# Kernel optimization log

Measured on AMD Instinct MI355X. Metric: run time of the kernel, lower is better.

The kernel has to match this reference:

```python
import jax, jax.numpy as jnp
import numpy as np

TOP_K = 8  # config.top_k


def setup_inputs() -> dict:
    key = jax.random.key(0)
    k1, k2 = jax.random.split(key)
    B, S, H, E = 4, 4096, 4096, 64
    x = jax.random.normal(k1, (B, S, H), dtype=jnp.float32)
    # nn.Linear(hidden_size, expert_num, bias=False) weight: [E, H]
    W = jax.random.normal(k2, (E, H), dtype=jnp.float32) / np.sqrt(H).astype(np.float32)
    return {"x": x, "W": W}


def reference(x, W):
    # gate linear: [B,S,H] @ [E,H]^T -> [B,S,E]
    logits = jnp.einsum('bsh,eh->bse', x, W)
    # top-k along experts
    topk_vals, indices = jax.lax.top_k(logits, TOP_K)  # [B,S,K]
    # scatter topk values into a -inf-filled tensor. Since the scattered src
    # values are exactly the logits at those indices, this equals masking.
    E = logits.shape[-1]
    mask = jax.nn.one_hot(indices, E, dtype=bool).any(axis=-2)  # [B,S,E]
    sparse_logits = jnp.where(mask, logits, -jnp.inf)
    sparse_probs = jax.nn.softmax(sparse_logits, axis=-1)  # [B,S,E]
    gate_logit = logits.reshape(-1, E)  # [B*S, E]
    return sparse_probs, indices, gate_logit
```

## Files before the change

### kernel.cpp

```cpp
#include <hip/hip_runtime.h>
#include <math.h>

#define H_DIM  4096
#define E_NUM  64
#define N_TOK  16384
#define TPB    64
#define KC     64
#define NCHUNK (H_DIM / KC)
#define TOPK   8

#define N_PROBS  (N_TOK * E_NUM)
#define N_IDX    (N_TOK * TOPK)
#define OFF_IDX  N_PROBS
#define OFF_GATE (N_PROBS + N_IDX)

__global__ __launch_bounds__(256, 1)
void gating_kernel(const float* __restrict__ x, const float* __restrict__ W,
                   float* __restrict__ out) {
  __shared__ union {
    float xs[2][KC][TPB];
    float lg[TPB][E_NUM + 1];
  } u;
  __shared__ float ws[2][KC][E_NUM];

  const int tid  = threadIdx.x;
  const int tok0 = blockIdx.x * TPB;
  const int tx   = tid & 15;
  const int ty   = tid >> 4;

  const float* xg = x + (size_t)tok0 * H_DIM;

  float4 xr[4], wr[4];

  auto gload = [&](int kb) {
#pragma unroll
    for (int p = 0; p < 4; ++p) {
      const int f4  = tid + 256 * p;
      const int row = f4 & 63;
      const int kq  = f4 >> 6;
      xr[p] = *(const float4*)(xg + row * H_DIM + kb + 4 * kq);
      wr[p] = *(const float4*)(W  + row * H_DIM + kb + 4 * kq);
    }
  };
  auto sstore = [&](int b) {
#pragma unroll
    for (int p = 0; p < 4; ++p) {
      const int f4  = tid + 256 * p;
      const int row = f4 & 63;
      const int k0  = (f4 >> 6) << 2;
      u.xs[b][k0 + 0][row] = xr[p].x;
      u.xs[b][k0 + 1][row] = xr[p].y;
      u.xs[b][k0 + 2][row] = xr[p].z;
      u.xs[b][k0 + 3][row] = xr[p].w;
      ws[b][k0 + 0][row] = wr[p].x;
      ws[b][k0 + 1][row] = wr[p].y;
      ws[b][k0 + 2][row] = wr[p].z;
      ws[b][k0 + 3][row] = wr[p].w;
    }
  };

  gload(0);
  sstore(0);
  __syncthreads();

  double accd[4][4];
#pragma unroll
  for (int i = 0; i < 4; ++i)
#pragma unroll
    for (int j = 0; j < 4; ++j) accd[i][j] = 0.0;

  for (int c = 0; c < NCHUNK; ++c) {
    if (c + 1 < NCHUNK) gload((c + 1) * KC);
    const int b = c & 1;

    float ca[4][4];
#pragma unroll
    for (int i = 0; i < 4; ++i)
#pragma unroll
      for (int j = 0; j < 4; ++j) ca[i][j] = 0.f;

#pragma unroll 8
    for (int k = 0; k < KC; ++k) {
      const float4 av = *(const float4*)&u.xs[b][k][4 * ty];
      const float4 bv = *(const float4*)&ws[b][k][4 * tx];
      const float a[4]  = {av.x, av.y, av.z, av.w};
      const float bb[4] = {bv.x, bv.y, bv.z, bv.w};
#pragma unroll
      for (int i = 0; i < 4; ++i)
#pragma unroll
        for (int j = 0; j < 4; ++j)
          ca[i][j] = fmaf(a[i], bb[j], ca[i][j]);
    }
#pragma unroll
    for (int i = 0; i < 4; ++i)
#pragma unroll
      for (int j = 0; j < 4; ++j) accd[i][j] += (double)ca[i][j];

    if (c + 1 < NCHUNK) {
      sstore((c + 1) & 1);
      __syncthreads();
    }
  }

  float acc[4][4];
#pragma unroll
  for (int i = 0; i < 4; ++i)
#pragma unroll
    for (int j = 0; j < 4; ++j) acc[i][j] = (float)accd[i][j];

  float* gate = out + OFF_GATE;
#pragma unroll
  for (int i = 0; i < 4; ++i) {
    const int t = 4 * ty + i;
    float4 v = make_float4(acc[i][0], acc[i][1], acc[i][2], acc[i][3]);
    *(float4*)(gate + (size_t)(tok0 + t) * E_NUM + 4 * tx) = v;
  }

  __syncthreads();
#pragma unroll
  for (int i = 0; i < 4; ++i)
#pragma unroll
    for (int j = 0; j < 4; ++j)
      u.lg[4 * ty + i][4 * tx + j] = acc[i][j];
  __syncthreads();

  if (tid < TPB) {
    const int t = tid;
    float vals[TOPK];
    int   idxs[TOPK];
#pragma unroll
    for (int p = 0; p < TOPK; ++p) {
      float best = -INFINITY;
      int   bi   = 0;
      for (int e = 0; e < E_NUM; ++e) {
        const float v = u.lg[t][e];
        if (v > best) { best = v; bi = e; }
      }
      vals[p] = best;
      idxs[p] = bi;
      u.lg[t][bi] = -INFINITY;
    }
    const float m = vals[0];
    float s = 0.f, pr[TOPK];
#pragma unroll
    for (int p = 0; p < TOPK; ++p) { pr[p] = __expf(vals[p] - m); s += pr[p]; }
    const float inv = 1.0f / s;
    for (int e = 0; e < E_NUM; ++e) u.lg[t][e] = 0.f;
#pragma unroll
    for (int p = 0; p < TOPK; ++p) u.lg[t][idxs[p]] = pr[p] * inv;

    float* oidx = out + OFF_IDX + (size_t)(tok0 + t) * TOPK;
#pragma unroll
    for (int p = 0; p < TOPK; ++p) oidx[p] = (float)idxs[p];
  }
  __syncthreads();

  float* oprob = out + (size_t)tok0 * E_NUM;
#pragma unroll
  for (int p = 0; p < 16; ++p) {
    const int f = tid + 256 * p;
    oprob[f] = u.lg[f >> 6][f & 63];
  }
}

extern "C" void kernel_launch(void* const* d_in, const int* in_sizes, int n_in,
                              void* d_out, int out_size, void* d_ws, size_t ws_size,
                              hipStream_t stream) {
  const float* x = (const float*)d_in[0];
  const float* W = (const float*)d_in[1];
  float* out = (float*)d_out;
  dim3 grid(N_TOK / TPB);
  dim3 block(256);
  gating_kernel<<<grid, block, 0, stream>>>(x, W, out);
}
```

Measured before the change: 453.7 us.

## Split K across two thread groups per block and reduce partials in shared memory

```diff
diff --git a/kernel.cpp b/kernel.cpp
--- a/kernel.cpp
+++ b/kernel.cpp
@@ -14,28 +14,30 @@
 #define OFF_IDX  N_PROBS
 #define OFF_GATE (N_PROBS + N_IDX)
 
-__global__ __launch_bounds__(256, 1)
+__global__ __launch_bounds__(512, 2)
 void gating_kernel(const float* __restrict__ x, const float* __restrict__ W,
                    float* __restrict__ out) {
   __shared__ union {
-    float xs[2][KC][TPB];
+    struct { float xs[2][KC][TPB]; float ws[2][KC][E_NUM]; } t;
+    struct { float pad[8192]; double b[16][256]; } r;
     float lg[TPB][E_NUM + 1];
   } u;
-  __shared__ float ws[2][KC][E_NUM];
 
   const int tid  = threadIdx.x;
+  const int g    = tid >> 8;
+  const int gtid = tid & 255;
   const int tok0 = blockIdx.x * TPB;
-  const int tx   = tid & 15;
-  const int ty   = tid >> 4;
+  const int tx   = gtid & 15;
+  const int ty   = gtid >> 4;
 
   const float* xg = x + (size_t)tok0 * H_DIM;
 
-  float4 xr[4], wr[4];
+  float4 xr[2], wr[2];
 
   auto gload = [&](int kb) {
 #pragma unroll
-    for (int p = 0; p < 4; ++p) {
-      const int f4  = tid + 256 * p;
+    for (int p = 0; p < 2; ++p) {
+      const int f4  = tid + 512 * p;
       const int row = f4 & 63;
       const int kq  = f4 >> 6;
       xr[p] = *(const float4*)(xg + row * H_DIM + kb + 4 * kq);
@@ -44,18 +46,18 @@
   };
   auto sstore = [&](int b) {
 #pragma unroll
-    for (int p = 0; p < 4; ++p) {
-      const int f4  = tid + 256 * p;
+    for (int p = 0; p < 2; ++p) {
+      const int f4  = tid + 512 * p;
       const int row = f4 & 63;
       const int k0  = (f4 >> 6) << 2;
-      u.xs[b][k0 + 0][row] = xr[p].x;
-      u.xs[b][k0 + 1][row] = xr[p].y;
-      u.xs[b][k0 + 2][row] = xr[p].z;
-      u.xs[b][k0 + 3][row] = xr[p].w;
-      ws[b][k0 + 0][row] = wr[p].x;
-      ws[b][k0 + 1][row] = wr[p].y;
-      ws[b][k0 + 2][row] = wr[p].z;
-      ws[b][k0 + 3][row] = wr[p].w;
+      u.t.xs[b][k0 + 0][row] = xr[p].x;
+      u.t.xs[b][k0 + 1][row] = xr[p].y;
+      u.t.xs[b][k0 + 2][row] = xr[p].z;
+      u.t.xs[b][k0 + 3][row] = xr[p].w;
+      u.t.ws[b][k0 + 0][row] = wr[p].x;
+      u.t.ws[b][k0 + 1][row] = wr[p].y;
+      u.t.ws[b][k0 + 2][row] = wr[p].z;
+      u.t.ws[b][k0 + 3][row] = wr[p].w;
     }
   };
 
@@ -64,25 +66,21 @@
   __syncthreads();
 
   double accd[4][4];
+  float  ca[4][4];
 #pragma unroll
   for (int i = 0; i < 4; ++i)
 #pragma unroll
-    for (int j = 0; j < 4; ++j) accd[i][j] = 0.0;
+    for (int j = 0; j < 4; ++j) { accd[i][j] = 0.0; ca[i][j] = 0.f; }
 
   for (int c = 0; c < NCHUNK; ++c) {
     if (c + 1 < NCHUNK) gload((c + 1) * KC);
     const int b = c & 1;
 
-    float ca[4][4];
-#pragma unroll
-    for (int i = 0; i < 4; ++i)
-#pragma unroll
-      for (int j = 0; j < 4; ++j) ca[i][j] = 0.f;
-
 #pragma unroll 8
-    for (int k = 0; k < KC; ++k) {
-      const float4 av = *(const float4*)&u.xs[b][k][4 * ty];
-      const float4 bv = *(const float4*)&ws[b][k][4 * tx];
+    for (int kk = 0; kk < KC / 2; ++kk) {
+      const int k = (g << 5) | kk;
+      const float4 av = *(const float4*)&u.t.xs[b][k][4 * ty];
+      const float4 bv = *(const float4*)&u.t.ws[b][k][4 * tx];
       const float a[4]  = {av.x, av.y, av.z, av.w};
       const float bb[4] = {bv.x, bv.y, bv.z, bv.w};
 #pragma unroll
@@ -91,37 +89,55 @@
         for (int j = 0; j < 4; ++j)
           ca[i][j] = fmaf(a[i], bb[j], ca[i][j]);
     }
+
+    if (c & 1) {
 #pragma unroll
-    for (int i = 0; i < 4; ++i)
+      for (int i = 0; i < 4; ++i)
 #pragma unroll
-      for (int j = 0; j < 4; ++j) accd[i][j] += (double)ca[i][j];
+        for (int j = 0; j < 4; ++j) {
+          accd[i][j] += (double)ca[i][j];
+          ca[i][j] = 0.f;
+        }
+    }
 
     if (c + 1 < NCHUNK) {
       sstore((c + 1) & 1);
       __syncthreads();
     }
   }
+  __syncthreads();
+
+  if (g == 1) {
+#pragma unroll
+    for (int i = 0; i < 4; ++i)
+#pragma unroll
+      for (int j = 0; j < 4; ++j)
+        u.r.b[4 * i + j][gtid] = accd[i][j];
+  }
+  __syncthreads();
 
   float acc[4][4];
+  if (g == 0) {
 #pragma unroll
-  for (int i = 0; i < 4; ++i)
+    for (int i = 0; i < 4; ++i)
 #pragma unroll
-    for (int j = 0; j < 4; ++j) acc[i][j] = (float)accd[i][j];
+      for (int j = 0; j < 4; ++j)
+        acc[i][j] = (float)(accd[i][j] + u.r.b[4 * i + j][gtid]);
 
-  float* gate = out + OFF_GATE;
+    float* gate = out + OFF_GATE;
 #pragma unroll
-  for (int i = 0; i < 4; ++i) {
-    const int t = 4 * ty + i;
-    float4 v = make_float4(acc[i][0], acc[i][1], acc[i][2], acc[i][3]);
-    *(float4*)(gate + (size_t)(tok0 + t) * E_NUM + 4 * tx) = v;
+    for (int i = 0; i < 4; ++i) {
+      const int t = 4 * ty + i;
+      float4 v = make_float4(acc[i][0], acc[i][1], acc[i][2], acc[i][3]);
+      *(float4*)(gate + (size_t)(tok0 + t) * E_NUM + 4 * tx) = v;
+    }
+
+#pragma unroll
+    for (int i = 0; i < 4; ++i)
+#pragma unroll
+      for (int j = 0; j < 4; ++j)
+        u.lg[4 * ty + i][4 * tx + j] = acc[i][j];
   }
-
-  __syncthreads();
-#pragma unroll
-  for (int i = 0; i < 4; ++i)
-#pragma unroll
-    for (int j = 0; j < 4; ++j)
-      u.lg[4 * ty + i][4 * tx + j] = acc[i][j];
   __syncthreads();
 
   if (tid < TPB) {
@@ -157,8 +173,8 @@
 
   float* oprob = out + (size_t)tok0 * E_NUM;
 #pragma unroll
-  for (int p = 0; p < 16; ++p) {
-    const int f = tid + 256 * p;
+  for (int p = 0; p < 8; ++p) {
+    const int f = tid + 512 * p;
     oprob[f] = u.lg[f >> 6][f & 63];
   }
 }
@@ -170,6 +186,6 @@
   const float* W = (const float*)d_in[1];
   float* out = (float*)d_out;
   dim3 grid(N_TOK / TPB);
-  dim3 block(256);
+  dim3 block(512);
   gating_kernel<<<grid, block, 0, stream>>>(x, W, out);
 }
```

New measurement: 507.3 us. 11.8% more time.

## Split GEMM along K with larger token tiles and separate reduce/top-k kernel

Applied to the files above, without the earlier changes.

```diff
diff --git a/kernel.cpp b/kernel.cpp
--- a/kernel.cpp
+++ b/kernel.cpp
@@ -1,13 +1,16 @@
 #include <hip/hip_runtime.h>
 #include <math.h>
 
-#define H_DIM  4096
-#define E_NUM  64
-#define N_TOK  16384
-#define TPB    64
-#define KC     64
-#define NCHUNK (H_DIM / KC)
-#define TOPK   8
+#define H_DIM   4096
+#define E_NUM   64
+#define N_TOK   16384
+#define TOPK    8
+
+#define TPB1    128
+#define KSPLIT  2
+#define KHALF   (H_DIM / KSPLIT)
+#define KC      64
+#define NCHUNK1 (KHALF / KC)
 
 #define N_PROBS  (N_TOK * E_NUM)
 #define N_IDX    (N_TOK * TOPK)
@@ -15,43 +18,55 @@
 #define OFF_GATE (N_PROBS + N_IDX)
 
 __global__ __launch_bounds__(256, 1)
-void gating_kernel(const float* __restrict__ x, const float* __restrict__ W,
-                   float* __restrict__ out) {
-  __shared__ union {
-    float xs[2][KC][TPB];
-    float lg[TPB][E_NUM + 1];
-  } u;
+void gemm_part(const float* __restrict__ x, const float* __restrict__ W,
+               float* __restrict__ out) {
+  __shared__ float xs[2][KC][TPB1];
   __shared__ float ws[2][KC][E_NUM];
 
-  const int tid  = threadIdx.x;
-  const int tok0 = blockIdx.x * TPB;
-  const int tx   = tid & 15;
-  const int ty   = tid >> 4;
-
-  const float* xg = x + (size_t)tok0 * H_DIM;
-
-  float4 xr[4], wr[4];
+  const int tid    = threadIdx.x;
+  const int tokgrp = blockIdx.x >> 1;
+  const int kpart  = blockIdx.x & 1;
+  const int tok0   = tokgrp * TPB1;
+  const int tx     = tid & 15;
+  const int ty     = tid >> 4;
+
+  const float* xg = x + (size_t)tok0 * H_DIM + (size_t)kpart * KHALF;
+  const float* wg = W + (size_t)kpart * KHALF;
+
+  float4 xr[8], wr[4];
 
   auto gload = [&](int kb) {
+#pragma unroll
+    for (int p = 0; p < 8; ++p) {
+      const int f4  = tid + 256 * p;
+      const int row = f4 & 127;
+      const int kq  = f4 >> 7;
+      xr[p] = *(const float4*)(xg + (size_t)row * H_DIM + kb + 4 * kq);
+    }
 #pragma unroll
     for (int p = 0; p < 4; ++p) {
       const int f4  = tid + 256 * p;
       const int row = f4 & 63;
       const int kq  = f4 >> 6;
-      xr[p] = *(const float4*)(xg + row * H_DIM + kb + 4 * kq);
-      wr[p] = *(const float4*)(W  + row * H_DIM + kb + 4 * kq);
+      wr[p] = *(const float4*)(wg + (size_t)row * H_DIM + kb + 4 * kq);
     }
   };
   auto sstore = [&](int b) {
 #pragma unroll
+    for (int p = 0; p < 8; ++p) {
+      const int f4  = tid + 256 * p;
+      const int row = f4 & 127;
+      const int k0  = (f4 >> 7) << 2;
+      xs[b][k0 + 0][row] = xr[p].x;
+      xs[b][k0 + 1][row] = xr[p].y;
+      xs[b][k0 + 2][row] = xr[p].z;
+      xs[b][k0 + 3][row] = xr[p].w;
+    }
+#pragma unroll
     for (int p = 0; p < 4; ++p) {
       const int f4  = tid + 256 * p;
       const int row = f4 & 63;
       const int k0  = (f4 >> 6) << 2;
-      u.xs[b][k0 + 0][row] = xr[p].x;
-      u.xs[b][k0 + 1][row] = xr[p].y;
-      u.xs[b][k0 + 2][row] = xr[p].z;
-      u.xs[b][k0 + 3][row] = xr[p].w;
       ws[b][k0 + 0][row] = wr[p].x;
       ws[b][k0 + 1][row] = wr[p].y;
       ws[b][k0 + 2][row] = wr[p].z;
@@ -63,68 +78,79 @@
   sstore(0);
   __syncthreads();
 
-  double accd[4][4];
-#pragma unroll
-  for (int i = 0; i < 4; ++i)
-#pragma unroll
-    for (int j = 0; j < 4; ++j) accd[i][j] = 0.0;
-
-  for (int c = 0; c < NCHUNK; ++c) {
-    if (c + 1 < NCHUNK) gload((c + 1) * KC);
+  double accd[8][4];
+  float  ca[8][4];
+#pragma unroll
+  for (int i = 0; i < 8; ++i)
+#pragma unroll
+    for (int j = 0; j < 4; ++j) { accd[i][j] = 0.0; ca[i][j] = 0.f; }
+
+  for (int c = 0; c < NCHUNK1; ++c) {
+    if (c + 1 < NCHUNK1) gload((c + 1) * KC);
     const int b = c & 1;
 
-    float ca[4][4];
-#pragma unroll
-    for (int i = 0; i < 4; ++i)
-#pragma unroll
-      for (int j = 0; j < 4; ++j) ca[i][j] = 0.f;
-
-#pragma unroll 8
+#pragma unroll 4
     for (int k = 0; k < KC; ++k) {
-      const float4 av = *(const float4*)&u.xs[b][k][4 * ty];
+      const float4 a0 = *(const float4*)&xs[b][k][8 * ty];
+      const float4 a1 = *(const float4*)&xs[b][k][8 * ty + 4];
       const float4 bv = *(const float4*)&ws[b][k][4 * tx];
-      const float a[4]  = {av.x, av.y, av.z, av.w};
+      const float a[8]  = {a0.x, a0.y, a0.z, a0.w, a1.x, a1.y, a1.z, a1.w};
       const float bb[4] = {bv.x, bv.y, bv.z, bv.w};
 #pragma unroll
-      for (int i = 0; i < 4; ++i)
+      for (int i = 0; i < 8; ++i)
 #pragma unroll
         for (int j = 0; j < 4; ++j)
           ca[i][j] = fmaf(a[i], bb[j], ca[i][j]);
     }
 #pragma unroll
-    for (int i = 0; i < 4; ++i)
-#pragma unroll
-      for (int j = 0; j < 4; ++j) accd[i][j] += (double)ca[i][j];
-
-    if (c + 1 < NCHUNK) {
+    for (int i = 0; i < 8; ++i)
+#pragma unroll
+      for (int j = 0; j < 4; ++j) { accd[i][j] += (double)ca[i][j]; ca[i][j] = 0.f; }
+
+    if (c + 1 < NCHUNK1) {
       sstore((c + 1) & 1);
       __syncthreads();
     }
   }
 
-  float acc[4][4];
-#pragma unroll
-  for (int i = 0; i < 4; ++i)
-#pragma unroll
-    for (int j = 0; j < 4; ++j) acc[i][j] = (float)accd[i][j];
+  float* pout = out + (kpart ? 0 : OFF_GATE);
+#pragma unroll
+  for (int i = 0; i < 8; ++i) {
+    const int t = 8 * ty + i;
+    float4 v = make_float4((float)accd[i][0], (float)accd[i][1],
+                           (float)accd[i][2], (float)accd[i][3]);
+    *(float4*)(pout + (size_t)(tok0 + t) * E_NUM + 4 * tx) = v;
+  }
+}
+
+__global__ __launch_bounds__(256, 1)
+void reduce_epilogue(float* __restrict__ out) {
+  __shared__ float lg[64][E_NUM + 1];
+
+  const int tid  = threadIdx.x;
+  const int tok0 = blockIdx.x * 64;
+  const int tx   = tid & 15;
+  const int ty   = tid >> 4;
 
   float* gate = out + OFF_GATE;
+  float* prob = out;
+
 #pragma unroll
   for (int i = 0; i < 4; ++i) {
     const int t = 4 * ty + i;
-    float4 v = make_float4(acc[i][0], acc[i][1], acc[i][2], acc[i][3]);
-    *(float4*)(gate + (size_t)(tok0 + t) * E_NUM + 4 * tx) = v;
-  }
-
+    const size_t off = (size_t)(tok0 + t) * E_NUM + 4 * tx;
+    const float4 pa = *(const float4*)(gate + off);
+    const float4 pb = *(const float4*)(prob + off);
+    float4 v = make_float4(pa.x + pb.x, pa.y + pb.y, pa.z + pb.z, pa.w + pb.w);
+    *(float4*)(gate + off) = v;
+    lg[t][4 * tx + 0] = v.x;
+    lg[t][4 * tx + 1] = v.y;
+    lg[t][4 * tx + 2] = v.z;
+    lg[t][4 * tx + 3] = v.w;
+  }
   __syncthreads();
-#pragma unroll
-  for (int i = 0; i < 4; ++i)
-#pragma unroll
-    for (int j = 0; j < 4; ++j)
-      u.lg[4 * ty + i][4 * tx + j] = acc[i][j];
-  __syncthreads();
-
-  if (tid < TPB) {
+
+  if (tid < 64) {
     const int t = tid;
     float vals[TOPK];
     int   idxs[TOPK];
@@ -133,21 +159,21 @@
       float best = -INFINITY;
       int   bi   = 0;
       for (int e = 0; e < E_NUM; ++e) {
-        const float v = u.lg[t][e];
+        const float v = lg[t][e];
         if (v > best) { best = v; bi = e; }
       }
       vals[p] = best;
       idxs[p] = bi;
-      u.lg[t][bi] = -INFINITY;
+      lg[t][bi] = -INFINITY;
     }
     const float m = vals[0];
     float s = 0.f, pr[TOPK];
 #pragma unroll
     for (int p = 0; p < TOPK; ++p) { pr[p] = __expf(vals[p] - m); s += pr[p]; }
     const float inv = 1.0f / s;
-    for (int e = 0; e < E_NUM; ++e) u.lg[t][e] = 0.f;
-#pragma unroll
-    for (int p = 0; p < TOPK; ++p) u.lg[t][idxs[p]] = pr[p] * inv;
+    for (int e = 0; e < E_NUM; ++e) lg[t][e] = 0.f;
+#pragma unroll
+    for (int p = 0; p < TOPK; ++p) lg[t][idxs[p]] = pr[p] * inv;
 
     float* oidx = out + OFF_IDX + (size_t)(tok0 + t) * TOPK;
 #pragma unroll
@@ -155,11 +181,11 @@
   }
   __syncthreads();
 
-  float* oprob = out + (size_t)tok0 * E_NUM;
+  float* oprob = prob + (size_t)tok0 * E_NUM;
 #pragma unroll
   for (int p = 0; p < 16; ++p) {
     const int f = tid + 256 * p;
-    oprob[f] = u.lg[f >> 6][f & 63];
+    oprob[f] = lg[f >> 6][f & 63];
   }
 }
 
@@ -169,7 +195,6 @@
   const float* x = (const float*)d_in[0];
   const float* W = (const float*)d_in[1];
   float* out = (float*)d_out;
-  dim3 grid(N_TOK / TPB);
-  dim3 block(256);
-  gating_kernel<<<grid, block, 0, stream>>>(x, W, out);
+  gemm_part<<<dim3(N_TOK / TPB1 * KSPLIT), dim3(256), 0, stream>>>(x, W, out);
+  reduce_epilogue<<<dim3(N_TOK / 64), dim3(256), 0, stream>>>(out);
 }
```

Result: slower. 466.5 us (+2.8%).

## Use bf16x3 split MFMA for gate GEMM with swizzled LDS tiles

Applied to the files above, without the earlier changes.

```diff
diff --git a/kernel.cpp b/kernel.cpp
--- a/kernel.cpp
+++ b/kernel.cpp
@@ -14,21 +14,52 @@
 #define OFF_IDX  N_PROBS
 #define OFF_GATE (N_PROBS + N_IDX)
 
+#define XH 0
+#define XM 1
+#define XL 2
+#define WH 3
+#define WM 4
+#define WL 5
+
+typedef __attribute__((ext_vector_type(8)))  short short8;
+typedef __attribute__((ext_vector_type(16))) float f32x16;
+
+__device__ __forceinline__ unsigned short bf_split(float v, float& rem) {
+  unsigned u  = __builtin_bit_cast(unsigned, v);
+  unsigned hb = (u + 0x7FFFu + ((u >> 16) & 1u)) & 0xFFFF0000u;
+  rem = v - __builtin_bit_cast(float, hb);
+  return (unsigned short)(hb >> 16);
+}
+__device__ __forceinline__ unsigned short bf_rne(float v) {
+  unsigned u = __builtin_bit_cast(unsigned, v);
+  return (unsigned short)((u + 0x7FFFu + ((u >> 16) & 1u)) >> 16);
+}
+
 __global__ __launch_bounds__(256, 1)
 void gating_kernel(const float* __restrict__ x, const float* __restrict__ W,
                    float* __restrict__ out) {
   __shared__ union {
-    float xs[2][KC][TPB];
+    unsigned short tiles[2][6][64][64];
     float lg[TPB][E_NUM + 1];
   } u;
-  __shared__ float ws[2][KC][E_NUM];
 
   const int tid  = threadIdx.x;
   const int tok0 = blockIdx.x * TPB;
-  const int tx   = tid & 15;
-  const int ty   = tid >> 4;
+  const int lane = tid & 63;
+  const int wid  = tid >> 6;
+  const int wm   = wid >> 1;
+  const int wn   = wid & 1;
+  const int l31  = lane & 31;
+  const int arow = 32 * wm + l31;
+  const int brow = 32 * wn + l31;
+  const int kloff = 16 * (lane >> 5);
 
   const float* xg = x + (size_t)tok0 * H_DIM;
+
+  auto sw = [&](int arr, int b, int row, int kbyte) -> void* {
+    return (char*)(&u.tiles[b][arr][0][0]) +
+           row * 128 + (kbyte ^ ((row & 7) << 4));
+  };
 
   float4 xr[4], wr[4];
 
@@ -36,26 +67,39 @@
 #pragma unroll
     for (int p = 0; p < 4; ++p) {
       const int f4  = tid + 256 * p;
-      const int row = f4 & 63;
-      const int kq  = f4 >> 6;
-      xr[p] = *(const float4*)(xg + row * H_DIM + kb + 4 * kq);
-      wr[p] = *(const float4*)(W  + row * H_DIM + kb + 4 * kq);
-    }
-  };
+      const int row = f4 >> 4;
+      const int kq  = f4 & 15;
+      xr[p] = *(const float4*)(xg + (size_t)row * H_DIM + kb + 4 * kq);
+      wr[p] = *(const float4*)(W  + (size_t)row * H_DIM + kb + 4 * kq);
+    }
+  };
+
+  auto cvt_store = [&](const float4& v, int abase, int b, int row, int kbyte) {
+    const float f[4] = {v.x, v.y, v.z, v.w};
+    unsigned short h[4], m[4], l[4];
+#pragma unroll
+    for (int i = 0; i < 4; ++i) {
+      float r1, r2;
+      h[i] = bf_split(f[i], r1);
+      m[i] = bf_split(r1, r2);
+      l[i] = bf_rne(r2);
+    }
+    ushort4 hv = {h[0], h[1], h[2], h[3]};
+    ushort4 mv = {m[0], m[1], m[2], m[3]};
+    ushort4 lv = {l[0], l[1], l[2], l[3]};
+    *(ushort4*)sw(abase + 0, b, row, kbyte) = hv;
+    *(ushort4*)sw(abase + 1, b, row, kbyte) = mv;
+    *(ushort4*)sw(abase + 2, b, row, kbyte) = lv;
+  };
+
   auto sstore = [&](int b) {
 #pragma unroll
     for (int p = 0; p < 4; ++p) {
-      const int f4  = tid + 256 * p;
-      const int row = f4 & 63;
-      const int k0  = (f4 >> 6) << 2;
-      u.xs[b][k0 + 0][row] = xr[p].x;
-      u.xs[b][k0 + 1][row] = xr[p].y;
-      u.xs[b][k0 + 2][row] = xr[p].z;
-      u.xs[b][k0 + 3][row] = xr[p].w;
-      ws[b][k0 + 0][row] = wr[p].x;
-      ws[b][k0 + 1][row] = wr[p].y;
-      ws[b][k0 + 2][row] = wr[p].z;
-      ws[b][k0 + 3][row] = wr[p].w;
+      const int f4    = tid + 256 * p;
+      const int row   = f4 >> 4;
+      const int kbyte = (f4 & 15) * 8;
+      cvt_store(xr[p], XH, b, row, kbyte);
+      cvt_store(wr[p], WH, b, row, kbyte);
     }
   };
 
@@ -63,38 +107,39 @@
   sstore(0);
   __syncthreads();
 
-  double accd[4][4];
-#pragma unroll
-  for (int i = 0; i < 4; ++i)
-#pragma unroll
-    for (int j = 0; j < 4; ++j) accd[i][j] = 0.0;
+  f32x16 accA, accB;
+  double accd[16];
+#pragma unroll
+  for (int r = 0; r < 16; ++r) { accA[r] = 0.f; accB[r] = 0.f; accd[r] = 0.0; }
 
   for (int c = 0; c < NCHUNK; ++c) {
     if (c + 1 < NCHUNK) gload((c + 1) * KC);
     const int b = c & 1;
 
-    float ca[4][4];
-#pragma unroll
-    for (int i = 0; i < 4; ++i)
-#pragma unroll
-      for (int j = 0; j < 4; ++j) ca[i][j] = 0.f;
-
-#pragma unroll 8
-    for (int k = 0; k < KC; ++k) {
-      const float4 av = *(const float4*)&u.xs[b][k][4 * ty];
-      const float4 bv = *(const float4*)&ws[b][k][4 * tx];
-      const float a[4]  = {av.x, av.y, av.z, av.w};
-      const float bb[4] = {bv.x, bv.y, bv.z, bv.w};
-#pragma unroll
-      for (int i = 0; i < 4; ++i)
-#pragma unroll
-        for (int j = 0; j < 4; ++j)
-          ca[i][j] = fmaf(a[i], bb[j], ca[i][j]);
-    }
-#pragma unroll
-    for (int i = 0; i < 4; ++i)
-#pragma unroll
-      for (int j = 0; j < 4; ++j) accd[i][j] += (double)ca[i][j];
+#pragma unroll
+    for (int kt = 0; kt < 4; ++kt) {
+      const int kb = kt * 32 + kloff;
+      const short8 ah = *(const short8*)sw(XH, b, arow, kb);
+      const short8 am = *(const short8*)sw(XM, b, arow, kb);
+      const short8 al = *(const short8*)sw(XL, b, arow, kb);
+      const short8 bh = *(const short8*)sw(WH, b, brow, kb);
+      const short8 bm = *(const short8*)sw(WM, b, brow, kb);
+      const short8 bl = *(const short8*)sw(WL, b, brow, kb);
+      accA = __builtin_amdgcn_mfma_f32_32x32x16_bf16(ah, bh, accA, 0, 0, 0);
+      accB = __builtin_amdgcn_mfma_f32_32x32x16_bf16(am, bm, accB, 0, 0, 0);
+      accA = __builtin_amdgcn_mfma_f32_32x32x16_bf16(am, bh, accA, 0, 0, 0);
+      accB = __builtin_amdgcn_mfma_f32_32x32x16_bf16(ah, bm, accB, 0, 0, 0);
+      accA = __builtin_amdgcn_mfma_f32_32x32x16_bf16(al, bh, accA, 0, 0, 0);
+      accB = __builtin_amdgcn_mfma_f32_32x32x16_bf16(ah, bl, accB, 0, 0, 0);
+    }
+
+    if ((c & 3) == 3) {
+#pragma unroll
+      for (int r = 0; r < 16; ++r) {
+        accd[r] += (double)accA[r] + (double)accB[r];
+        accA[r] = 0.f; accB[r] = 0.f;
+      }
+    }
 
     if (c + 1 < NCHUNK) {
       sstore((c + 1) & 1);
@@ -102,26 +147,22 @@
     }
   }
 
-  float acc[4][4];
-#pragma unroll
-  for (int i = 0; i < 4; ++i)
-#pragma unroll
-    for (int j = 0; j < 4; ++j) acc[i][j] = (float)accd[i][j];
-
+  __syncthreads();
+
+  const int rb = 4 * (lane >> 5);
   float* gate = out + OFF_GATE;
 #pragma unroll
-  for (int i = 0; i < 4; ++i) {
-    const int t = 4 * ty + i;
-    float4 v = make_float4(acc[i][0], acc[i][1], acc[i][2], acc[i][3]);
-    *(float4*)(gate + (size_t)(tok0 + t) * E_NUM + 4 * tx) = v;
-  }
-
-  __syncthreads();
-#pragma unroll
-  for (int i = 0; i < 4; ++i)
-#pragma unroll
-    for (int j = 0; j < 4; ++j)
-      u.lg[4 * ty + i][4 * tx + j] = acc[i][j];
+  for (int q = 0; q < 4; ++q)
+#pragma unroll
+    for (int j = 0; j < 4; ++j) {
+      const int reg   = 4 * q + j;
+      const int row32 = j + 8 * q + rb;
+      const float v   = (float)accd[reg];
+      const int trow  = 32 * wm + row32;
+      const int e     = 32 * wn + l31;
+      gate[(size_t)(tok0 + trow) * E_NUM + e] = v;
+      u.lg[trow][e] = v;
+    }
   __syncthreads();
 
   if (tid < TPB) {
```

New measurement: 405.9 us. 10.5% less time.
